# Kernel tuning notes

Hardware: AMD Instinct MI355X
Metric: run time of the kernel (lower is better)

## Reference

```python
import jax, jax.numpy as jnp
import numpy as np

B = 16384          # tokens
H = 2048           # hidden_size
E = 8              # num_experts
K = 2              # top-k
HF = H // 4        # expert bottleneck dim


def setup_inputs() -> dict:
    key = jax.random.key(0)
    k0, k1, k2, k3 = jax.random.split(key, 4)
    scale = lambda kk, shape, fan: jax.random.normal(kk, shape, jnp.float32) * (1.0 / np.sqrt(fan))
    x = jax.random.normal(k0, (B, H), jnp.float32)
    W1 = scale(k1, (E, H, HF), H)      # experts[e][0].weight (transposed)
    b1 = jnp.zeros((E, HF), jnp.float32)
    W2 = scale(k2, (E, HF), HF)        # experts[e][2].weight (out dim 1, no bias)
    Wg = scale(k3, (H, E), H)          # gate.weight (transposed)
    bg = jnp.zeros((E,), jnp.float32)
    return {"x": x, "W1": W1, "b1": b1, "W2": W2, "Wg": Wg, "bg": bg}


def reference(x, W1, b1, W2, Wg, bg):
    # Gating (eval mode: no noise branch)
    logits = x @ Wg + bg                                  # [B, E]
    top_w, top_i = jax.lax.top_k(logits, K)               # [B, K]
    w = jax.nn.softmax(top_w, axis=-1)                    # [B, K]
    # Scatter top-k softmax weights into dense combine weights [B, E];
    # unselected experts get weight 0, so the dense all-expert compute
    # below is mathematically identical to the masked dispatch loop.
    combine = jnp.zeros_like(logits).at[jnp.arange(x.shape[0])[:, None], top_i].add(w)
    # All-expert MLP: Linear -> exact GELU -> Linear(->1, no bias)
    h = jax.nn.gelu(jnp.einsum('bh,ehf->bef', x, W1) + b1, approximate=False)  # [B, E, HF]
    o = jnp.einsum('bef,ef->be', h, W2)                   # [B, E]
    final_scores = jnp.sum(combine * o, axis=-1, keepdims=True)  # [B, 1]
    return final_scores, logits
```

## Files before the change

kernel.cpp:

```cpp
#include <hip/hip_runtime.h>
#include <math.h>

#define B_TOK 16384
#define H_DIM 2048
#define NE    8
#define TOPK  2
#define HFD   512

#define BK 64
#define NKSTEP (H_DIM / BK)
#define PTMAX 129
#define PROWS 33792

static constexpr size_t OFF_COUNTS = 0;
static constexpr size_t OFF_CBASE  = 128;
static constexpr size_t OFF_BUCKET = 1024;
static constexpr size_t OFF_WSLOT  = 525312;
static constexpr size_t OFF_ROUTE  = 656384;
static constexpr size_t OFF_INV    = 721920;
static constexpr size_t OFF_WGT    = 1u << 20;
static constexpr size_t OFF_P4     = 1572864;
static constexpr size_t OFF_W1Q    = 4u << 20;
static constexpr size_t OFF_XB     = 20971520;

typedef short bfrag __attribute__((ext_vector_type(8)));
typedef float facc  __attribute__((ext_vector_type(16)));

__device__ inline unsigned short f2bf(float f) {
    union { float f; unsigned u; } v; v.f = f;
    unsigned r = v.u + 0x7FFFu + ((v.u >> 16) & 1u);
    return (unsigned short)(r >> 16);
}
__device__ inline unsigned pack2(float lo, float hi) {
    return (unsigned)f2bf(lo) | ((unsigned)f2bf(hi) << 16);
}

__device__ __forceinline__ void gload_lds16(const void* g, void* l) {
    __builtin_amdgcn_global_load_lds(
        (const __attribute__((address_space(1))) unsigned int*)g,
        (__attribute__((address_space(3))) unsigned int*)l, 16, 0, 0);
}

__global__ __launch_bounds__(256)
void wg_transpose_kernel(const float* __restrict__ Wg,
                         float* __restrict__ WgT)
{
    const int t = threadIdx.x;
    #pragma unroll
    for (int rep = 0; rep < H_DIM / 256; ++rep) {
        const int h = rep * 256 + t;
        const float4 a = *reinterpret_cast<const float4*>(Wg + (size_t)h * NE);
        const float4 b = *reinterpret_cast<const float4*>(Wg + (size_t)h * NE + 4);
        #pragma unroll
        for (int rr = 0; rr < 8; ++rr) {
            float* W = WgT + (size_t)rr * (NE * H_DIM);
            W[0 * H_DIM + h] = a.x;  W[1 * H_DIM + h] = a.y;
            W[2 * H_DIM + h] = a.z;  W[3 * H_DIM + h] = a.w;
            W[4 * H_DIM + h] = b.x;  W[5 * H_DIM + h] = b.y;
            W[6 * H_DIM + h] = b.z;  W[7 * H_DIM + h] = b.w;
        }
    }
}

__global__ __launch_bounds__(256)
void prep_w1_kernel(const float* __restrict__ W1,
                    unsigned short* __restrict__ W1q)
{
    const int e     = blockIdx.x >> 5;
    const int kstep = blockIdx.x & 31;
    const int tid   = threadIdx.x;

    const float* src = W1 + ((size_t)e * H_DIM + kstep * BK) * HFD;

    #pragma unroll
    for (int slot = 0; slot < 8; ++slot) {
        #pragma unroll
        for (int half = 0; half < 2; ++half) {
            const int f  = half * 256 + tid;
            const int fq = f >> 7;
            const int fl = f & 127;
            float v[8];
            #pragma unroll
            for (int j = 0; j < 8; ++j)
                v[j] = src[(size_t)(slot * 8 + j) * HFD + f];
            uint4 p;
            p.x = pack2(v[0], v[1]); p.y = pack2(v[2], v[3]);
            p.z = pack2(v[4], v[5]); p.w = pack2(v[6], v[7]);
            *reinterpret_cast<uint4*>(
                W1q + ((size_t)((e * 4 + fq) * 32 + kstep)) * 8192
                    + (slot * 128 + fl) * 8) = p;
        }
    }
}

__global__ __launch_bounds__(256)
void gate_logits_kernel(const float* __restrict__ x,
                        const float* __restrict__ WgT,
                        const float* __restrict__ bg,
                        float* __restrict__ out_logits,
                        float* __restrict__ wslot,
                        int*   __restrict__ route,
                        unsigned short* __restrict__ xb)
{
    __shared__ float Wlds[NE * H_DIM];

    const int tid = threadIdx.x;
    const float* Wsrc = WgT + (size_t)(blockIdx.x & 7) * (NE * H_DIM);
    #pragma unroll
    for (int i = 0; i < (NE * H_DIM) / (256 * 4); ++i) {
        const int idx = (i * 256 + tid) * 4;
        *reinterpret_cast<float4*>(&Wlds[idx]) =
            *reinterpret_cast<const float4*>(Wsrc + idx);
    }
    __syncthreads();

    const int w = tid >> 6, l = tid & 63;
    const int tbase = blockIdx.x * 64 + w * 16;

    for (int pass = 0; pass < 4; ++pass) {
        const int t0 = tbase + pass * 4;
        float acc[4][NE];
        #pragma unroll
        for (int j = 0; j < 4; ++j)
            #pragma unroll
            for (int e = 0; e < NE; ++e) acc[j][e] = 0.f;

        for (int i = 0; i < 8; ++i) {
            const int h = i * 256 + 4 * l;
            float4 xv[4];
            #pragma unroll
            for (int j = 0; j < 4; ++j)
                xv[j] = *reinterpret_cast<const float4*>(
                    x + (size_t)(t0 + j) * H_DIM + h);
            #pragma unroll
            for (int j = 0; j < 4; ++j) {
                uint2 pk;
                pk.x = pack2(xv[j].x, xv[j].y);
                pk.y = pack2(xv[j].z, xv[j].w);
                *reinterpret_cast<uint2*>(xb + (size_t)(t0 + j) * H_DIM + h) = pk;
            }
            #pragma unroll
            for (int e = 0; e < NE; ++e) {
                const float4 wv = *reinterpret_cast<const float4*>(&Wlds[e * H_DIM + h]);
                #pragma unroll
                for (int j = 0; j < 4; ++j)
                    acc[j][e] += xv[j].x * wv.x + xv[j].y * wv.y
                               + xv[j].z * wv.z + xv[j].w * wv.w;
            }
        }

        #pragma unroll
        for (int j = 0; j < 4; ++j)
            #pragma unroll
            for (int e = 0; e < NE; ++e)
                #pragma unroll
                for (int off = 32; off > 0; off >>= 1)
                    acc[j][e] += __shfl_xor(acc[j][e], off, 64);

        if (l == 0) {
            #pragma unroll
            for (int j = 0; j < 4; ++j) {
                const int tok = t0 + j;
                float lg[NE];
                #pragma unroll
                for (int e = 0; e < NE; ++e) lg[e] = acc[j][e] + bg[e];

                float4* lo = reinterpret_cast<float4*>(out_logits + (size_t)tok * NE);
                lo[0] = make_float4(lg[0], lg[1], lg[2], lg[3]);
                lo[1] = make_float4(lg[4], lg[5], lg[6], lg[7]);

                int i0 = 0; float v0 = lg[0];
                #pragma unroll
                for (int e = 1; e < NE; ++e)
                    if (lg[e] > v0) { v0 = lg[e]; i0 = e; }
                int i1 = -1; float v1 = -3.4e38f;
                #pragma unroll
                for (int e = 0; e < NE; ++e)
                    if (e != i0 && lg[e] > v1) { v1 = lg[e]; i1 = e; }

                const float w0 = 1.f / (1.f + expf(v1 - v0));
                wslot[tok * 2]     = w0;
                wslot[tok * 2 + 1] = 1.f - w0;
                route[tok] = i0 | (i1 << 8);
            }
        }
    }
}

__global__ __launch_bounds__(1024)
void route_kernel(const int* __restrict__ route,
                  int* __restrict__ counts,
                  int* __restrict__ bucket)
{
    __shared__ int lcnt[NE];
    __shared__ int lbase[NE];
    const int tid = threadIdx.x;
    const int tok = blockIdx.x * 1024 + tid;

    if (tid < NE) lcnt[tid] = 0;
    __syncthreads();

    const int rt = route[tok];
    const int i0 = rt & 255;
    const int i1 = rt >> 8;
    const int r0 = atomicAdd(&lcnt[i0], 1);
    const int r1 = atomicAdd(&lcnt[i1], 1);
    __syncthreads();

    if (tid < NE) lbase[tid] = atomicAdd(&counts[tid], lcnt[tid]);
    __syncthreads();

    bucket[i0 * B_TOK + lbase[i0] + r0] = tok * 2;
    bucket[i1 * B_TOK + lbase[i1] + r1] = tok * 2 + 1;
}

__global__ void prefix_kernel(const int* __restrict__ counts,
                              int* __restrict__ cbase)
{
    if (threadIdx.x == 0 && blockIdx.x == 0) {
        int acc = 0;
        for (int e = 0; e < NE; ++e) {
            const int cp = ((counts[e] + 127) >> 7) << 7;
            cbase[e]      = acc;
            cbase[NE + e] = cp;
            acc += cp;
        }
    }
}

__global__ __launch_bounds__(256)
void invfill_kernel(const int* __restrict__ bucket,
                    const int* __restrict__ counts,
                    const int* __restrict__ cbase,
                    int* __restrict__ inv)
{
    const int e   = blockIdx.x & 7;
    const int pos = (blockIdx.x >> 3) * 256 + threadIdx.x;
    if (pos < counts[e]) inv[bucket[e * B_TOK + pos]] = cbase[e] + pos;
}

__global__ __launch_bounds__(256, 4)
void expert_mfma_kernel(const unsigned short* __restrict__ xb,
                        const unsigned short* __restrict__ W1q,
                        const float* __restrict__ b1,
                        const float* __restrict__ W2,
                        const int* __restrict__ counts,
                        const int* __restrict__ cbase,
                        const int* __restrict__ bucket,
                        float* __restrict__ P4)
{
    const int e  = blockIdx.x & 7;
    const int r  = blockIdx.x >> 3;
    const int fq = r & 3;
    const int pt = r >> 2;
    const int n  = counts[e];
    const int pos0 = pt * 128;
    if (pos0 >= n) return;
    const int nt = min(128, n - pos0);
    const int cb = cbase[e];

    __shared__ unsigned short Albs[8192];
    __shared__ unsigned short Blds[8192];
    __shared__ float o_part[2][128];

    const int tid = threadIdx.x;
    const int w   = tid >> 6;
    const int l   = tid & 63;
    const int lo5 = l & 31;
    const int hi  = l >> 5;
    const int wm  = w & 1;
    const int wn  = w >> 1;

    const unsigned short* Aimg = W1q + (size_t)((e * 4 + fq) * 32) * 8192;

    const unsigned short* xsrc0, *xsrc1, *xsrc2, *xsrc3;
    {
        const int u0 = 0 * 256 + tid, u1 = 1 * 256 + tid,
                  u2 = 2 * 256 + tid, u3 = 3 * 256 + tid;
        const int r0 = u0 >> 3, r1 = u1 >> 3, r2 = u2 >> 3, r3 = u3 >> 3;
        const int t0 = bucket[e * B_TOK + min(pos0 + r0, n - 1)] >> 1;
        const int t1 = bucket[e * B_TOK + min(pos0 + r1, n - 1)] >> 1;
        const int t2 = bucket[e * B_TOK + min(pos0 + r2, n - 1)] >> 1;
        const int t3 = bucket[e * B_TOK + min(pos0 + r3, n - 1)] >> 1;
        xsrc0 = xb + (size_t)t0 * H_DIM + (((u0 & 7) ^ (r0 & 7)) * 8);
        xsrc1 = xb + (size_t)t1 * H_DIM + (((u1 & 7) ^ (r1 & 7)) * 8);
        xsrc2 = xb + (size_t)t2 * H_DIM + (((u2 & 7) ^ (r2 & 7)) * 8);
        xsrc3 = xb + (size_t)t3 * H_DIM + (((u3 & 7) ^ (r3 & 7)) * 8);
    }

    facc acc00, acc01, acc10, acc11;
    #pragma unroll
    for (int q = 0; q < 16; ++q) {
        acc00[q] = 0.f; acc01[q] = 0.f; acc10[q] = 0.f; acc11[q] = 0.f;
    }

    for (int kk = 0; kk < NKSTEP; ++kk) {
        const unsigned short* as = Aimg + (size_t)kk * 8192;
        {
            const int o0 = (0 * 256 + tid) * 8, o1 = (1 * 256 + tid) * 8;
            const int o2 = (2 * 256 + tid) * 8, o3 = (3 * 256 + tid) * 8;
            gload_lds16(as + o0, Albs + o0);
            gload_lds16(as + o1, Albs + o1);
            gload_lds16(as + o2, Albs + o2);
            gload_lds16(as + o3, Albs + o3);
            gload_lds16(xsrc0 + kk * BK, Blds + o0);
            gload_lds16(xsrc1 + kk * BK, Blds + o1);
            gload_lds16(xsrc2 + kk * BK, Blds + o2);
            gload_lds16(xsrc3 + kk * BK, Blds + o3);
        }
        __syncthreads();

        #pragma unroll
        for (int s = 0; s < 4; ++s) {
            const int slot  = s * 2 + hi;
            const int chunk = slot ^ (lo5 & 7);
            const bfrag a0 = *reinterpret_cast<const bfrag*>(
                &Albs[(slot * 128 + wm * 64 + lo5) * 8]);
            const bfrag a1 = *reinterpret_cast<const bfrag*>(
                &Albs[(slot * 128 + wm * 64 + 32 + lo5) * 8]);
            const bfrag b0 = *reinterpret_cast<const bfrag*>(
                &Blds[((wn * 64 + lo5) * 8 + chunk) * 8]);
            const bfrag b1v = *reinterpret_cast<const bfrag*>(
                &Blds[((wn * 64 + 32 + lo5) * 8 + chunk) * 8]);
            acc00 = __builtin_amdgcn_mfma_f32_32x32x16_bf16(a0, b0,  acc00, 0, 0, 0);
            acc01 = __builtin_amdgcn_mfma_f32_32x32x16_bf16(a0, b1v, acc01, 0, 0, 0);
            acc10 = __builtin_amdgcn_mfma_f32_32x32x16_bf16(a1, b0,  acc10, 0, 0, 0);
            acc11 = __builtin_amdgcn_mfma_f32_32x32x16_bf16(a1, b1v, acc11, 0, 0, 0);
        }
        __syncthreads();
    }

    const float* b1e = b1 + e * HFD + fq * 128;
    const float* W2e = W2 + e * HFD + fq * 128;
    const float kInvSqrt2 = 0.70710678118654752f;

    float po0 = 0.f, po1 = 0.f;
    #pragma unroll
    for (int mb = 0; mb < 2; ++mb) {
        const int base = wm * 64 + mb * 32 + 4 * hi;
        #pragma unroll
        for (int q = 0; q < 16; ++q) {
            const int frow = base + (q & 3) + 8 * (q >> 2);
            const float bv = b1e[frow];
            const float wv = W2e[frow];
            const float h0 = (mb ? acc10[q] : acc00[q]) + bv;
            const float h1 = (mb ? acc11[q] : acc01[q]) + bv;
            po0 += 0.5f * h0 * (1.f + erff(h0 * kInvSqrt2)) * wv;
            po1 += 0.5f * h1 * (1.f + erff(h1 * kInvSqrt2)) * wv;
        }
    }
    po0 += __shfl_xor(po0, 32, 64);
    po1 += __shfl_xor(po1, 32, 64);

    if (hi == 0) {
        o_part[wm][wn * 64 + lo5]      = po0;
        o_part[wm][wn * 64 + 32 + lo5] = po1;
    }
    __syncthreads();

    if (tid < nt)
        P4[(size_t)fq * PROWS + cb + pos0 + tid] =
            o_part[0][tid] + o_part[1][tid];
}

__global__ __launch_bounds__(256)
void combine_kernel(const int* __restrict__ inv,
                    const float* __restrict__ P4,
                    const float* __restrict__ wslot,
                    float* __restrict__ out_scores)
{
    const int t = blockIdx.x * 256 + threadIdx.x;
    if (t >= B_TOK) return;
    const int g0 = inv[2 * t];
    const int g1 = inv[2 * t + 1];
    const float s0 = ((P4[g0] + P4[PROWS + g0]) + P4[2 * PROWS + g0])
                   + P4[3 * PROWS + g0];
    const float s1 = ((P4[g1] + P4[PROWS + g1]) + P4[2 * PROWS + g1])
                   + P4[3 * PROWS + g1];
    out_scores[t] = wslot[2 * t] * s0 + wslot[2 * t + 1] * s1;
}

extern "C" void kernel_launch(void* const* d_in, const int* in_sizes, int n_in,
                              void* d_out, int out_size, void* d_ws, size_t ws_size,
                              hipStream_t stream)
{
    const float* x  = (const float*)d_in[0];
    const float* W1 = (const float*)d_in[1];
    const float* b1 = (const float*)d_in[2];
    const float* W2 = (const float*)d_in[3];
    const float* Wg = (const float*)d_in[4];
    const float* bg = (const float*)d_in[5];

    float* out        = (float*)d_out;
    float* out_scores = out;
    float* out_logits = out + B_TOK;

    char* ws = (char*)d_ws;
    int*            counts = (int*)           (ws + OFF_COUNTS);
    int*            cbase  = (int*)           (ws + OFF_CBASE);
    int*            bucket = (int*)           (ws + OFF_BUCKET);
    float*          wslot  = (float*)         (ws + OFF_WSLOT);
    int*            route  = (int*)           (ws + OFF_ROUTE);
    int*            inv    = (int*)           (ws + OFF_INV);
    float*          WgT    = (float*)         (ws + OFF_WGT);
    float*          P4     = (float*)         (ws + OFF_P4);
    unsigned short* W1q    = (unsigned short*)(ws + OFF_W1Q);
    unsigned short* xb     = (unsigned short*)(ws + OFF_XB);

    hipMemsetAsync(counts, 0, NE * sizeof(int), stream);

    wg_transpose_kernel<<<1, 256, 0, stream>>>(Wg, WgT);

    prep_w1_kernel<<<NE * NKSTEP, 256, 0, stream>>>(W1, W1q);

    gate_logits_kernel<<<B_TOK / 64, 256, 0, stream>>>(x, WgT, bg, out_logits,
                                                       wslot, route, xb);

    route_kernel<<<B_TOK / 1024, 1024, 0, stream>>>(route, counts, bucket);

    prefix_kernel<<<1, 64, 0, stream>>>(counts, cbase);

    invfill_kernel<<<NE * (B_TOK / 256), 256, 0, stream>>>(bucket, counts,
                                                           cbase, inv);

    expert_mfma_kernel<<<NE * 4 * PTMAX, 256, 0, stream>>>(
        xb, W1q, b1, W2, counts, cbase, bucket, P4);

    combine_kernel<<<B_TOK / 256, 256, 0, stream>>>(inv, P4, wslot, out_scores);
}
```

Before: 246.6 us.

## Double-buffer LDS tiles with BK=32 to overlap global loads with MFMA

Halves the K-tile to 32 and adds two LDS buffers for the weight and gathered-token tiles, so the next tile's async global-to-LDS loads are issued before computing the current one. Explicit vmcnt waits and raw s_barrier replace __syncthreads, and the W1 prep layout and LDS swizzle are changed to match the smaller tile. The aim is to hide global load latency behind the matrix cores. In exchange the kernel runs twice as many K iterations with barriers, and the hand-written waitcnt/barrier synchronisation carries a risk of LDS races.

After: 256.0 us. 3.8% more time.

```diff
diff --git a/kernel.cpp b/kernel.cpp
--- a/kernel.cpp
+++ b/kernel.cpp
@@ -7,7 +7,7 @@
 #define TOPK  2
 #define HFD   512
 
-#define BK 64
+#define BK 32
 #define NKSTEP (H_DIM / BK)
 #define PTMAX 129
 #define PROWS 33792
@@ -66,14 +66,14 @@
 void prep_w1_kernel(const float* __restrict__ W1,
                     unsigned short* __restrict__ W1q)
 {
-    const int e     = blockIdx.x >> 5;
-    const int kstep = blockIdx.x & 31;
+    const int e     = blockIdx.x >> 6;
+    const int kstep = blockIdx.x & 63;
     const int tid   = threadIdx.x;
 
     const float* src = W1 + ((size_t)e * H_DIM + kstep * BK) * HFD;
 
     #pragma unroll
-    for (int slot = 0; slot < 8; ++slot) {
+    for (int slot = 0; slot < 4; ++slot) {
         #pragma unroll
         for (int half = 0; half < 2; ++half) {
             const int f  = half * 256 + tid;
@@ -87,7 +87,7 @@
             p.x = pack2(v[0], v[1]); p.y = pack2(v[2], v[3]);
             p.z = pack2(v[4], v[5]); p.w = pack2(v[6], v[7]);
             *reinterpret_cast<uint4*>(
-                W1q + ((size_t)((e * 4 + fq) * 32 + kstep)) * 8192
+                W1q + ((size_t)((e * 4 + fq) * 64 + kstep)) * 4096
                     + (slot * 128 + fl) * 8) = p;
         }
     }
@@ -259,8 +259,8 @@
     const int nt = min(128, n - pos0);
     const int cb = cbase[e];
 
-    __shared__ unsigned short Albs[8192];
-    __shared__ unsigned short Blds[8192];
+    __shared__ unsigned short Abuf[2][4096];
+    __shared__ unsigned short Bbuf[2][4096];
     __shared__ float o_part[2][128];
 
     const int tid = threadIdx.x;
@@ -271,22 +271,18 @@
     const int wm  = w & 1;
     const int wn  = w >> 1;
 
-    const unsigned short* Aimg = W1q + (size_t)((e * 4 + fq) * 32) * 8192;
-
-    const unsigned short* xsrc0, *xsrc1, *xsrc2, *xsrc3;
-    {
-        const int u0 = 0 * 256 + tid, u1 = 1 * 256 + tid,
-                  u2 = 2 * 256 + tid, u3 = 3 * 256 + tid;
-        const int r0 = u0 >> 3, r1 = u1 >> 3, r2 = u2 >> 3, r3 = u3 >> 3;
-        const int t0 = bucket[e * B_TOK + min(pos0 + r0, n - 1)] >> 1;
-        const int t1 = bucket[e * B_TOK + min(pos0 + r1, n - 1)] >> 1;
-        const int t2 = bucket[e * B_TOK + min(pos0 + r2, n - 1)] >> 1;
-        const int t3 = bucket[e * B_TOK + min(pos0 + r3, n - 1)] >> 1;
-        xsrc0 = xb + (size_t)t0 * H_DIM + (((u0 & 7) ^ (r0 & 7)) * 8);
-        xsrc1 = xb + (size_t)t1 * H_DIM + (((u1 & 7) ^ (r1 & 7)) * 8);
-        xsrc2 = xb + (size_t)t2 * H_DIM + (((u2 & 7) ^ (r2 & 7)) * 8);
-        xsrc3 = xb + (size_t)t3 * H_DIM + (((u3 & 7) ^ (r3 & 7)) * 8);
-    }
+    const unsigned short* Aimg = W1q + (size_t)((e * 4 + fq) * 64) * 4096;
+
+    const int u0 = tid, u1 = 256 + tid;
+    const int r0 = u0 >> 2, r1 = u1 >> 2;
+    const int t0 = bucket[e * B_TOK + min(pos0 + r0, n - 1)] >> 1;
+    const int t1 = bucket[e * B_TOK + min(pos0 + r1, n - 1)] >> 1;
+    const unsigned short* xsrc0 =
+        xb + (size_t)t0 * H_DIM + (((u0 & 3) ^ ((r0 >> 1) & 3)) * 8);
+    const unsigned short* xsrc1 =
+        xb + (size_t)t1 * H_DIM + (((u1 & 3) ^ ((r1 >> 1) & 3)) * 8);
+    const int o0 = u0 * 8;
+    const int o1 = u1 * 8;
 
     facc acc00, acc01, acc10, acc11;
     #pragma unroll
@@ -294,41 +290,49 @@
         acc00[q] = 0.f; acc01[q] = 0.f; acc10[q] = 0.f; acc11[q] = 0.f;
     }
 
+    #define STAGE(KK, BUF) do {                                                \
+        const unsigned short* as_ = Aimg + (size_t)(KK) * 4096;                \
+        gload_lds16(as_ + o0, &Abuf[BUF][o0]);                                 \
+        gload_lds16(as_ + o1, &Abuf[BUF][o1]);                                 \
+        gload_lds16(xsrc0 + (KK) * BK, &Bbuf[BUF][o0]);                        \
+        gload_lds16(xsrc1 + (KK) * BK, &Bbuf[BUF][o1]);                        \
+    } while (0)
+
+    STAGE(0, 0);
+
     for (int kk = 0; kk < NKSTEP; ++kk) {
-        const unsigned short* as = Aimg + (size_t)kk * 8192;
-        {
-            const int o0 = (0 * 256 + tid) * 8, o1 = (1 * 256 + tid) * 8;
-            const int o2 = (2 * 256 + tid) * 8, o3 = (3 * 256 + tid) * 8;
-            gload_lds16(as + o0, Albs + o0);
-            gload_lds16(as + o1, Albs + o1);
-            gload_lds16(as + o2, Albs + o2);
-            gload_lds16(as + o3, Albs + o3);
-            gload_lds16(xsrc0 + kk * BK, Blds + o0);
-            gload_lds16(xsrc1 + kk * BK, Blds + o1);
-            gload_lds16(xsrc2 + kk * BK, Blds + o2);
-            gload_lds16(xsrc3 + kk * BK, Blds + o3);
-        }
-        __syncthreads();
-
-        #pragma unroll
-        for (int s = 0; s < 4; ++s) {
-            const int slot  = s * 2 + hi;
-            const int chunk = slot ^ (lo5 & 7);
+        const int cur = kk & 1;
+        if (kk < NKSTEP - 1) {
+            STAGE(kk + 1, cur ^ 1);
+            asm volatile("s_waitcnt vmcnt(4)" ::: "memory");
+        } else {
+            asm volatile("s_waitcnt vmcnt(0)" ::: "memory");
+        }
+        __builtin_amdgcn_s_barrier();
+
+        #pragma unroll
+        for (int s = 0; s < 2; ++s) {
+            const int slot = s * 2 + hi;
+            const int row0 = wn * 64 + lo5;
+            const int row1 = row0 + 32;
+            const int c0 = slot ^ ((row0 >> 1) & 3);
+            const int c1 = slot ^ ((row1 >> 1) & 3);
             const bfrag a0 = *reinterpret_cast<const bfrag*>(
-                &Albs[(slot * 128 + wm * 64 + lo5) * 8]);
+                &Abuf[cur][(slot * 128 + wm * 64 + lo5) * 8]);
             const bfrag a1 = *reinterpret_cast<const bfrag*>(
-                &Albs[(slot * 128 + wm * 64 + 32 + lo5) * 8]);
+                &Abuf[cur][(slot * 128 + wm * 64 + 32 + lo5) * 8]);
             const bfrag b0 = *reinterpret_cast<const bfrag*>(
-                &Blds[((wn * 64 + lo5) * 8 + chunk) * 8]);
+                &Bbuf[cur][(row0 * 4 + c0) * 8]);
             const bfrag b1v = *reinterpret_cast<const bfrag*>(
-                &Blds[((wn * 64 + 32 + lo5) * 8 + chunk) * 8]);
+                &Bbuf[cur][(row1 * 4 + c1) * 8]);
             acc00 = __builtin_amdgcn_mfma_f32_32x32x16_bf16(a0, b0,  acc00, 0, 0, 0);
             acc01 = __builtin_amdgcn_mfma_f32_32x32x16_bf16(a0, b1v, acc01, 0, 0, 0);
             acc10 = __builtin_amdgcn_mfma_f32_32x32x16_bf16(a1, b0,  acc10, 0, 0, 0);
             acc11 = __builtin_amdgcn_mfma_f32_32x32x16_bf16(a1, b1v, acc11, 0, 0, 0);
         }
-        __syncthreads();
-    }
+        __builtin_amdgcn_s_barrier();
+    }
+    #undef STAGE
 
     const float* b1e = b1 + e * HFD + fq * 128;
     const float* W2e = W2 + e * HFD + fq * 128;
```
